# Kernel tuning notes

Hardware: AMD Instinct MI355X
Metric: run time of the kernel (lower is better)

Reference implementation:

```python
import jax, jax.numpy as jnp
import numpy as np

N_CLASSES = 256
PER_CLASS = 128
N_SUPPORT = 5
N_QUERY = PER_CLASS - N_SUPPORT  # 123
N_VIEW = 2
D = 384
N = N_CLASSES * PER_CLASS  # 32768


def setup_inputs() -> dict:
    key = jax.random.key(0)
    k1, k2 = jax.random.split(key, 2)
    reps = jax.random.normal(k1, (N, N_VIEW, D), dtype=jnp.float32)
    # block-sorted labels: class c occupies rows [c*PER_CLASS, (c+1)*PER_CLASS)
    labels = (jnp.arange(N, dtype=jnp.int32) // PER_CLASS).astype(jnp.int32)
    return {"reps": reps, "labels": labels}


def reference(reps, labels):
    # labels are block-sorted per class, so the original's
    # labels.eq(c).nonzero()[:n_support] / [n_support:] gathers are static reshapes.
    reps_r = reps.reshape(N_CLASSES, PER_CLASS, N_VIEW, D)
    # class-mean prototypes over the support set: [C, V, D]
    prototypes = reps_r[:, :N_SUPPORT].mean(axis=1)
    # query samples: [C*N_QUERY, V, D]
    queries = reps_r[:, N_SUPPORT:].reshape(N_CLASSES * N_QUERY, N_VIEW, D)

    x2 = jnp.sum(queries * queries, axis=-1)            # [n, V]
    y2 = jnp.sum(prototypes * prototypes, axis=-1)      # [m, V]
    xy = jnp.einsum('nvd,mvd->nmv', queries, prototypes)  # [n, m, V]
    dists = x2[:, None, :] + y2[None, :, :] - 2.0 * xy

    # log_softmax over the prototype (class) axis
    log_p_y = jax.nn.log_softmax(-dists, axis=1)
    log_p_y = log_p_y.reshape(N_CLASSES, N_QUERY, N_CLASSES, N_VIEW)

    # gather the true-class log-prob for each query / view
    cls = jnp.arange(N_CLASSES)
    correct = log_p_y[cls, :, cls, :]  # [C, N_QUERY, V]
    loss = -correct.mean()
    return loss
```

## Files before the change

### kernel.cpp

```cpp
#include <hip/hip_runtime.h>
#include <hip/hip_bf16.h>
#include <math.h>

#define NCLS 256
#define PER_CLASS 128
#define NSUP 5
#define NQRY 123
#define NVIEW 2
#define DD 384
#define NQ_TOT (NCLS * NQRY)
#define BM 128
#define BK 32
#define NKT (DD / BK)
#define QS 40
#define PS 32

typedef __attribute__((ext_vector_type(8))) short short8;
typedef __attribute__((ext_vector_type(4))) float floatx4;

union FragU { uint4 u; short8 s; };
union PkU { __hip_bfloat162 b2; unsigned int u; };

__device__ __forceinline__ unsigned int cvt2bf(float lo, float hi) {
    PkU p;
    p.b2 = __float22bfloat162_rn(make_float2(lo, hi));
    return p.u;
}

__device__ __forceinline__ void gll16(const ushort* g, ushort* l) {
    __builtin_amdgcn_global_load_lds(
        (const __attribute__((address_space(1))) unsigned int*)g,
        (__attribute__((address_space(3))) unsigned int*)l, 16, 0, 0);
}

#define BARRIER() asm volatile("s_waitcnt lgkmcnt(0)\n\ts_barrier" ::: "memory")
#define WAITVM(n) asm volatile("s_waitcnt vmcnt(" #n ")" ::: "memory")

__global__ __launch_bounds__(384) void proto_kernel(const float* __restrict__ reps,
                                                    ushort* __restrict__ pbf,
                                                    float* __restrict__ y2,
                                                    float* __restrict__ out) {
    __shared__ float wp[6];
    const int b = blockIdx.x;
    const int c = b & 255, v = b >> 8;
    const int d = threadIdx.x;
    if (b == 0 && d == 0) out[0] = 0.f;
    const float* p = reps + ((size_t)(c * PER_CLASS) * NVIEW + v) * DD + d;
    float s = 0.f;
#pragma unroll
    for (int k = 0; k < NSUP; ++k) s += p[(size_t)k * NVIEW * DD];
    s *= 0.2f;
    __hip_bfloat16 h = __float2bfloat16(s);
    pbf[(size_t)b * DD + d] = *reinterpret_cast<ushort*>(&h);
    float q = s * s;
#pragma unroll
    for (int o = 1; o < 64; o <<= 1) q += __shfl_xor(q, o);
    if ((d & 63) == 0) wp[d >> 6] = q;
    __syncthreads();
    if (d == 0) y2[b] = wp[0] + wp[1] + wp[2] + wp[3] + wp[4] + wp[5];
}

__global__ __launch_bounds__(512, 4) void main_kernel(const float* __restrict__ reps,
                                                      const ushort* __restrict__ pbf,
                                                      const float* __restrict__ y2g,
                                                      float* __restrict__ out) {
    __shared__ ushort q_lds[2][BM * QS];
    __shared__ ushort p_lds[2][NCLS * PS];

    const int t = threadIdx.x;
    const int v = blockIdx.y;
    const int q0 = blockIdx.x * BM;
    const int wave = t >> 6;
    const int lane = t & 63;
    const int col = lane & 15;
    const int quad = lane >> 4;
    const int wm = wave >> 2;
    const int wn = wave & 3;

    const int sq = t >> 2;
    const int f8 = (t & 3) * 8;
    const int nq = q0 + sq;
    const float* qsrc = reps +
        (size_t)((nq / NQRY) * PER_CLASS + NSUP + (nq % NQRY)) * (NVIEW * DD) + v * DD + f8;

    const ushort* psrc = pbf + (size_t)(v * NCLS + wave * 32 + (lane >> 2)) * DD
                             + (((lane & 3) ^ ((lane >> 3) & 3)) << 3);

    const int sP = (col >> 1) & 3;
    const int pbase = (wn * 64 + col) * PS + ((quad ^ sP) << 3);

    floatx4 acc[4][4];
#pragma unroll
    for (int mt = 0; mt < 4; ++mt)
#pragma unroll
        for (int nt = 0; nt < 4; ++nt) acc[mt][nt] = (floatx4)0.f;

    float4 qfA[2], qfB[2];

#define LOADQ(kt, R)                                                               \
    do {                                                                           \
        R[0] = *(const float4*)(qsrc + (kt) * BK);                                 \
        R[1] = *(const float4*)(qsrc + (kt) * BK + 4);                             \
    } while (0)

#define GLLP(kt, b)                                                                \
    do {                                                                           \
        gll16(psrc + (kt) * BK, &p_lds[b][wave * 1024]);                           \
        gll16(psrc + 16 * DD + (kt) * BK, &p_lds[b][wave * 1024 + 512]);           \
    } while (0)

#define STAGEQ(b, R)                                                               \
    do {                                                                           \
        uint4 w;                                                                   \
        w.x = cvt2bf(R[0].x, R[0].y); w.y = cvt2bf(R[0].z, R[0].w);                \
        w.z = cvt2bf(R[1].x, R[1].y); w.w = cvt2bf(R[1].z, R[1].w);                \
        *(uint4*)&q_lds[b][sq * QS + f8] = w;                                      \
    } while (0)

#define COMPUTE(b)                                                                 \
    do {                                                                           \
        short8 af[4];                                                              \
        _Pragma("unroll") for (int mt = 0; mt < 4; ++mt) {                         \
            FragU f;                                                               \
            f.u = *(const uint4*)&q_lds[b][(wm * 64 + mt * 16 + col) * QS + quad * 8]; \
            af[mt] = f.s;                                                          \
        }                                                                          \
        _Pragma("unroll") for (int nt = 0; nt < 4; ++nt) {                         \
            FragU bb;                                                              \
            bb.u = *(const uint4*)&p_lds[b][pbase + nt * 16 * PS];                 \
            _Pragma("unroll") for (int mt = 0; mt < 4; ++mt)                       \
                acc[mt][nt] = __builtin_amdgcn_mfma_f32_16x16x32_bf16(af[mt], bb.s, acc[mt][nt], 0, 0, 0); \
        }                                                                          \
    } while (0)

    LOADQ(0, qfA); GLLP(0, 0);
    LOADQ(1, qfB); GLLP(1, 1);
    WAITVM(4);
    STAGEQ(0, qfA);
    BARRIER();

#pragma unroll
    for (int kt = 0; kt < NKT; ++kt) {
        COMPUTE(kt & 1);
        if (kt == NKT - 1) break;
        BARRIER();
        if (kt < NKT - 2) {
            if ((kt & 1) == 0) { LOADQ(kt + 2, qfA); } else { LOADQ(kt + 2, qfB); }
            GLLP(kt + 2, kt & 1);
            WAITVM(4);
        } else {
            WAITVM(0);
        }
        if ((kt & 1) == 0) STAGEQ(1, qfB); else STAGEQ(0, qfA);
        BARRIER();
    }

    __syncthreads();
    float* eplds = (float*)&p_lds[0][0];
    float (*pmx)[4] = (float(*)[4])eplds;
    float (*pse)[4] = (float(*)[4])(eplds + 512);
    float* wred = eplds + 1024;

    float y2c[4];
#pragma unroll
    for (int nt = 0; nt < 4; ++nt) y2c[nt] = y2g[v * NCLS + wn * 64 + nt * 16 + col];

    float corr = 0.f;
#pragma unroll
    for (int mt = 0; mt < 4; ++mt) {
#pragma unroll
        for (int r = 0; r < 4; ++r) {
            const int qloc = wm * 64 + mt * 16 + quad * 4 + r;
            const int n = q0 + qloc;
            const int cn = n / NQRY;
            float s[4];
            float mx = -1e30f;
#pragma unroll
            for (int nt = 0; nt < 4; ++nt) {
                s[nt] = 2.f * acc[mt][nt][r] - y2c[nt];
                mx = fmaxf(mx, s[nt]);
                if (cn == wn * 64 + nt * 16 + col) corr += s[nt];
            }
#pragma unroll
            for (int o = 1; o < 16; o <<= 1) mx = fmaxf(mx, __shfl_xor(mx, o));
            float e = 0.f;
#pragma unroll
            for (int nt = 0; nt < 4; ++nt) e += __expf(s[nt] - mx);
#pragma unroll
            for (int o = 1; o < 16; o <<= 1) e += __shfl_xor(e, o);
            if (col == 0) { pmx[qloc][wn] = mx; pse[qloc][wn] = e; }
        }
    }
#pragma unroll
    for (int o = 1; o < 64; o <<= 1) corr += __shfl_xor(corr, o);
    if (lane == 0) wred[wave] = corr;
    __syncthreads();

    float lval = 0.f;
    if (t < BM) {
        float m0 = pmx[t][0], m1 = pmx[t][1], m2 = pmx[t][2], m3 = pmx[t][3];
        float M = fmaxf(fmaxf(m0, m1), fmaxf(m2, m3));
        float E = pse[t][0] * __expf(m0 - M) + pse[t][1] * __expf(m1 - M) +
                  pse[t][2] * __expf(m2 - M) + pse[t][3] * __expf(m3 - M);
        lval = M + __logf(E);
    }
#pragma unroll
    for (int o = 1; o < 64; o <<= 1) lval += __shfl_xor(lval, o);
    if (lane == 0) wred[8 + wave] = lval;
    __syncthreads();

    if (t == 0) {
        float tot = (wred[8] + wred[9] + wred[10] + wred[11] +
                     wred[12] + wred[13] + wred[14] + wred[15]) -
                    (wred[0] + wred[1] + wred[2] + wred[3] +
                     wred[4] + wred[5] + wred[6] + wred[7]);
        atomicAdd(out, tot * (1.f / (float)(NQ_TOT * NVIEW)));
    }
}

extern "C" void kernel_launch(void* const* d_in, const int* in_sizes, int n_in,
                              void* d_out, int out_size, void* d_ws, size_t ws_size,
                              hipStream_t stream) {
    const float* reps = (const float*)d_in[0];
    float* ws = (float*)d_ws;
    ushort* pbf = (ushort*)ws;
    float* y2 = (float*)(pbf + NVIEW * NCLS * DD);
    float* out = (float*)d_out;

    proto_kernel<<<dim3(NVIEW * NCLS), dim3(DD), 0, stream>>>(reps, pbf, y2, out);
    main_kernel<<<dim3(NQ_TOT / BM, NVIEW), dim3(512), 0, stream>>>(reps, pbf, y2, out);
}
```

Baseline: 165.5 us.

## Pre-convert queries to bf16 and triple-buffer tiles with direct global-to-LDS loads

The prep kernel now also converts every query row from fp32 to a packed bf16 buffer in workspace, alongside computing prototypes. The main kernel loads both query and prototype tiles straight into LDS with global_load_lds and a three-stage buffer, removing the register staging and the conversion from the GEMM loop and one barrier per iteration. In exchange it adds an extra full write and read of the bf16 query copy. It also drops the LDS padding and swizzle, which may cause bank conflicts, and uses more LDS per block, which may lower occupancy.

```diff
diff --git a/kernel.cpp b/kernel.cpp
--- a/kernel.cpp
+++ b/kernel.cpp
@@ -12,8 +12,9 @@
 #define BM 128
 #define BK 32
 #define NKT (DD / BK)
-#define QS 40
-#define PS 32
+#define NPROTO (NVIEW * NCLS)
+#define QCONV_BLOCKS 1536
+#define CHUNKS (NVIEW * NQ_TOT * (DD / 8))
 
 typedef __attribute__((ext_vector_type(8))) short short8;
 typedef __attribute__((ext_vector_type(4))) float floatx4;
@@ -36,36 +37,57 @@
 #define BARRIER() asm volatile("s_waitcnt lgkmcnt(0)\n\ts_barrier" ::: "memory")
 #define WAITVM(n) asm volatile("s_waitcnt vmcnt(" #n ")" ::: "memory")
 
-__global__ __launch_bounds__(384) void proto_kernel(const float* __restrict__ reps,
-                                                    ushort* __restrict__ pbf,
-                                                    float* __restrict__ y2,
-                                                    float* __restrict__ out) {
+__global__ __launch_bounds__(384) void prep_kernel(const float* __restrict__ reps,
+                                                   ushort* __restrict__ pbf,
+                                                   float* __restrict__ y2,
+                                                   ushort* __restrict__ qbf,
+                                                   float* __restrict__ out) {
     __shared__ float wp[6];
-    const int b = blockIdx.x;
-    const int c = b & 255, v = b >> 8;
-    const int d = threadIdx.x;
-    if (b == 0 && d == 0) out[0] = 0.f;
-    const float* p = reps + ((size_t)(c * PER_CLASS) * NVIEW + v) * DD + d;
-    float s = 0.f;
-#pragma unroll
-    for (int k = 0; k < NSUP; ++k) s += p[(size_t)k * NVIEW * DD];
-    s *= 0.2f;
-    __hip_bfloat16 h = __float2bfloat16(s);
-    pbf[(size_t)b * DD + d] = *reinterpret_cast<ushort*>(&h);
-    float q = s * s;
-#pragma unroll
-    for (int o = 1; o < 64; o <<= 1) q += __shfl_xor(q, o);
-    if ((d & 63) == 0) wp[d >> 6] = q;
-    __syncthreads();
-    if (d == 0) y2[b] = wp[0] + wp[1] + wp[2] + wp[3] + wp[4] + wp[5];
-}
-
-__global__ __launch_bounds__(512, 4) void main_kernel(const float* __restrict__ reps,
+    const int t = threadIdx.x;
+    if (blockIdx.x < NPROTO) {
+        const int b = blockIdx.x;
+        const int c = b & 255, v = b >> 8;
+        if (b == 0 && t == 0) out[0] = 0.f;
+        const float* p = reps + ((size_t)(c * PER_CLASS) * NVIEW + v) * DD + t;
+        float s = 0.f;
+#pragma unroll
+        for (int k = 0; k < NSUP; ++k) s += p[(size_t)k * NVIEW * DD];
+        s *= 0.2f;
+        __hip_bfloat16 h = __float2bfloat16(s);
+        pbf[(size_t)b * DD + t] = *reinterpret_cast<ushort*>(&h);
+        float q = s * s;
+#pragma unroll
+        for (int o = 1; o < 64; o <<= 1) q += __shfl_xor(q, o);
+        if ((t & 63) == 0) wp[t >> 6] = q;
+        __syncthreads();
+        if (t == 0) y2[b] = wp[0] + wp[1] + wp[2] + wp[3] + wp[4] + wp[5];
+    } else {
+        const int g0 = (blockIdx.x - NPROTO) * 384 + t;
+        for (int g = g0; g < CHUNKS; g += QCONV_BLOCKS * 384) {
+            const int row = g / 48;
+            const int d8 = g - row * 48;
+            const int v = row / NQ_TOT;
+            const int nq = row - v * NQ_TOT;
+            const int c = nq / NQRY;
+            const int qi = nq - c * NQRY;
+            const float* src = reps +
+                (size_t)((c * PER_CLASS + NSUP + qi) * NVIEW + v) * DD + d8 * 8;
+            const float4 a = *(const float4*)src;
+            const float4 b4 = *(const float4*)(src + 4);
+            uint4 w;
+            w.x = cvt2bf(a.x, a.y);  w.y = cvt2bf(a.z, a.w);
+            w.z = cvt2bf(b4.x, b4.y); w.w = cvt2bf(b4.z, b4.w);
+            *(uint4*)(qbf + (size_t)row * DD + d8 * 8) = w;
+        }
+    }
+}
+
+__global__ __launch_bounds__(512, 4) void main_kernel(const ushort* __restrict__ qbf,
                                                       const ushort* __restrict__ pbf,
                                                       const float* __restrict__ y2g,
                                                       float* __restrict__ out) {
-    __shared__ ushort q_lds[2][BM * QS];
-    __shared__ ushort p_lds[2][NCLS * PS];
+    __shared__ ushort q_lds[3][BM * 32];
+    __shared__ ushort p_lds[3][NCLS * 32];
 
     const int t = threadIdx.x;
     const int v = blockIdx.y;
@@ -77,17 +99,14 @@
     const int wm = wave >> 2;
     const int wn = wave & 3;
 
-    const int sq = t >> 2;
-    const int f8 = (t & 3) * 8;
-    const int nq = q0 + sq;
-    const float* qsrc = reps +
-        (size_t)((nq / NQRY) * PER_CLASS + NSUP + (nq % NQRY)) * (NVIEW * DD) + v * DD + f8;
-
-    const ushort* psrc = pbf + (size_t)(v * NCLS + wave * 32 + (lane >> 2)) * DD
-                             + (((lane & 3) ^ ((lane >> 3) & 3)) << 3);
-
-    const int sP = (col >> 1) & 3;
-    const int pbase = (wn * 64 + col) * PS + ((quad ^ sP) << 3);
+    const ushort* qsrc = qbf + (size_t)(v * NQ_TOT + q0 + wave * 16 + (lane >> 2)) * DD
+                             + (lane & 3) * 8;
+    const ushort* psrc0 = pbf + (size_t)(v * NCLS + wave * 16 + (lane >> 2)) * DD
+                              + (lane & 3) * 8;
+    const ushort* psrc1 = psrc0 + (size_t)128 * DD;
+
+    const int qdst = wave * 512;
+    const int pdst1 = 4096 + wave * 512;
 
     floatx4 acc[4][4];
 #pragma unroll
@@ -95,26 +114,11 @@
 #pragma unroll
         for (int nt = 0; nt < 4; ++nt) acc[mt][nt] = (floatx4)0.f;
 
-    float4 qfA[2], qfB[2];
-
-#define LOADQ(kt, R)                                                               \
+#define GLLT(kt, b)                                                                \
     do {                                                                           \
-        R[0] = *(const float4*)(qsrc + (kt) * BK);                                 \
-        R[1] = *(const float4*)(qsrc + (kt) * BK + 4);                             \
-    } while (0)
-
-#define GLLP(kt, b)                                                                \
-    do {                                                                           \
-        gll16(psrc + (kt) * BK, &p_lds[b][wave * 1024]);                           \
-        gll16(psrc + 16 * DD + (kt) * BK, &p_lds[b][wave * 1024 + 512]);           \
-    } while (0)
-
-#define STAGEQ(b, R)                                                               \
-    do {                                                                           \
-        uint4 w;                                                                   \
-        w.x = cvt2bf(R[0].x, R[0].y); w.y = cvt2bf(R[0].z, R[0].w);                \
-        w.z = cvt2bf(R[1].x, R[1].y); w.w = cvt2bf(R[1].z, R[1].w);                \
-        *(uint4*)&q_lds[b][sq * QS + f8] = w;                                      \
+        gll16(qsrc + (kt) * BK, &q_lds[b][qdst]);                                  \
+        gll16(psrc0 + (kt) * BK, &p_lds[b][qdst]);                                 \
+        gll16(psrc1 + (kt) * BK, &p_lds[b][pdst1]);                                \
     } while (0)
 
 #define COMPUTE(b)                                                                 \
@@ -122,41 +126,34 @@
         short8 af[4];                                                              \
         _Pragma("unroll") for (int mt = 0; mt < 4; ++mt) {                         \
             FragU f;                                                               \
-            f.u = *(const uint4*)&q_lds[b][(wm * 64 + mt * 16 + col) * QS + quad * 8]; \
+            f.u = *(const uint4*)&q_lds[b][(wm * 64 + mt * 16 + col) * 32 + quad * 8]; \
             af[mt] = f.s;                                                          \
         }                                                                          \
         _Pragma("unroll") for (int nt = 0; nt < 4; ++nt) {                         \
             FragU bb;                                                              \
-            bb.u = *(const uint4*)&p_lds[b][pbase + nt * 16 * PS];                 \
+            bb.u = *(const uint4*)&p_lds[b][(wn * 64 + nt * 16 + col) * 32 + quad * 8]; \
             _Pragma("unroll") for (int mt = 0; mt < 4; ++mt)                       \
                 acc[mt][nt] = __builtin_amdgcn_mfma_f32_16x16x32_bf16(af[mt], bb.s, acc[mt][nt], 0, 0, 0); \
         }                                                                          \
     } while (0)
 
-    LOADQ(0, qfA); GLLP(0, 0);
-    LOADQ(1, qfB); GLLP(1, 1);
-    WAITVM(4);
-    STAGEQ(0, qfA);
+    GLLT(0, 0);
+    GLLT(1, 1);
+    GLLT(2, 2);
+    WAITVM(6);
     BARRIER();
 
 #pragma unroll
     for (int kt = 0; kt < NKT; ++kt) {
-        COMPUTE(kt & 1);
+        COMPUTE(kt % 3);
         if (kt == NKT - 1) break;
+        if (kt + 2 < NKT) { WAITVM(3); } else { WAITVM(0); }
         BARRIER();
-        if (kt < NKT - 2) {
-            if ((kt & 1) == 0) { LOADQ(kt + 2, qfA); } else { LOADQ(kt + 2, qfB); }
-            GLLP(kt + 2, kt & 1);
-            WAITVM(4);
-        } else {
-            WAITVM(0);
-        }
-        if ((kt & 1) == 0) STAGEQ(1, qfB); else STAGEQ(0, qfA);
-        BARRIER();
+        if (kt + 3 < NKT) GLLT(kt + 3, kt % 3);
     }
 
     __syncthreads();
-    float* eplds = (float*)&p_lds[0][0];
+    float* eplds = (float*)&q_lds[0][0];
     float (*pmx)[4] = (float(*)[4])eplds;
     float (*pse)[4] = (float(*)[4])(eplds + 512);
     float* wred = eplds + 1024;
@@ -222,11 +219,11 @@
                               void* d_out, int out_size, void* d_ws, size_t ws_size,
                               hipStream_t stream) {
     const float* reps = (const float*)d_in[0];
-    float* ws = (float*)d_ws;
-    ushort* pbf = (ushort*)ws;
+    ushort* pbf = (ushort*)d_ws;
     float* y2 = (float*)(pbf + NVIEW * NCLS * DD);
+    ushort* qbf = (ushort*)(y2 + NVIEW * NCLS);
     float* out = (float*)d_out;
 
-    proto_kernel<<<dim3(NVIEW * NCLS), dim3(DD), 0, stream>>>(reps, pbf, y2, out);
-    main_kernel<<<dim3(NQ_TOT / BM, NVIEW), dim3(512), 0, stream>>>(reps, pbf, y2, out);
-}
+    prep_kernel<<<dim3(NPROTO + QCONV_BLOCKS), dim3(384), 0, stream>>>(reps, pbf, y2, qbf, out);
+    main_kernel<<<dim3(NQ_TOT / BM, NVIEW), dim3(512), 0, stream>>>(qbf, pbf, y2, out);
+}
```

Result: slower. 186.5 us (+12.7%).

## Stage the full query tile into LDS upfront with swizzled layout

Applied to the files above, without the earlier changes.

Each block now loads its whole 128x384 query tile once at the start (24 float4 loads per thread), converts it to bf16 and writes it into a single large LDS buffer with an XOR swizzle. This replaces the per-k-step double-buffered query staging, so the main loop only streams prototype tiles. The aim is to issue all query loads early with high memory-level parallelism and remove per-iteration conversion and LDS-store work. In exchange LDS use grows to about 96KB plus the prototype buffers and register pressure rises, so occupancy drops (launch bounds lowered from 4 to 2) and the query loads are no longer overlapped with the MFMA compute.

```diff
diff --git a/kernel.cpp b/kernel.cpp
--- a/kernel.cpp
+++ b/kernel.cpp
@@ -12,7 +12,6 @@
 #define BM 128
 #define BK 32
 #define NKT (DD / BK)
-#define QS 40
 #define PS 32
 
 typedef __attribute__((ext_vector_type(8))) short short8;
@@ -60,11 +59,11 @@
     if (d == 0) y2[b] = wp[0] + wp[1] + wp[2] + wp[3] + wp[4] + wp[5];
 }
 
-__global__ __launch_bounds__(512, 4) void main_kernel(const float* __restrict__ reps,
+__global__ __launch_bounds__(512, 2) void main_kernel(const float* __restrict__ reps,
                                                       const ushort* __restrict__ pbf,
                                                       const float* __restrict__ y2g,
                                                       float* __restrict__ out) {
-    __shared__ ushort q_lds[2][BM * QS];
+    __shared__ ushort q_lds[NKT * BM * 32];
     __shared__ ushort p_lds[2][NCLS * PS];
 
     const int t = threadIdx.x;
@@ -77,31 +76,11 @@
     const int wm = wave >> 2;
     const int wn = wave & 3;
 
-    const int sq = t >> 2;
-    const int f8 = (t & 3) * 8;
-    const int nq = q0 + sq;
-    const float* qsrc = reps +
-        (size_t)((nq / NQRY) * PER_CLASS + NSUP + (nq % NQRY)) * (NVIEW * DD) + v * DD + f8;
-
     const ushort* psrc = pbf + (size_t)(v * NCLS + wave * 32 + (lane >> 2)) * DD
                              + (((lane & 3) ^ ((lane >> 3) & 3)) << 3);
 
     const int sP = (col >> 1) & 3;
     const int pbase = (wn * 64 + col) * PS + ((quad ^ sP) << 3);
-
-    floatx4 acc[4][4];
-#pragma unroll
-    for (int mt = 0; mt < 4; ++mt)
-#pragma unroll
-        for (int nt = 0; nt < 4; ++nt) acc[mt][nt] = (floatx4)0.f;
-
-    float4 qfA[2], qfB[2];
-
-#define LOADQ(kt, R)                                                               \
-    do {                                                                           \
-        R[0] = *(const float4*)(qsrc + (kt) * BK);                                 \
-        R[1] = *(const float4*)(qsrc + (kt) * BK + 4);                             \
-    } while (0)
 
 #define GLLP(kt, b)                                                                \
     do {                                                                           \
@@ -109,49 +88,73 @@
         gll16(psrc + 16 * DD + (kt) * BK, &p_lds[b][wave * 1024 + 512]);           \
     } while (0)
 
-#define STAGEQ(b, R)                                                               \
-    do {                                                                           \
-        uint4 w;                                                                   \
-        w.x = cvt2bf(R[0].x, R[0].y); w.y = cvt2bf(R[0].z, R[0].w);                \
-        w.z = cvt2bf(R[1].x, R[1].y); w.w = cvt2bf(R[1].z, R[1].w);                \
-        *(uint4*)&q_lds[b][sq * QS + f8] = w;                                      \
-    } while (0)
-
-#define COMPUTE(b)                                                                 \
+    GLLP(0, 0);
+    GLLP(1, 1);
+
+    {
+        const int qrow = t >> 2;
+        const int qp = t & 3;
+        const int nq = q0 + qrow;
+        const float* qsrc = reps +
+            (size_t)((nq / NQRY) * PER_CLASS + NSUP + (nq % NQRY)) * (NVIEW * DD) +
+            v * DD + qp * 96;
+        const int swzq = (qrow >> 1) & 3;
+
+        float4 A[24];
+#pragma unroll
+        for (int i = 0; i < 24; ++i) A[i] = *(const float4*)(qsrc + i * 4);
+#pragma unroll
+        for (int g = 0; g < 3; ++g) {
+            const int kt = qp * 3 + g;
+#pragma unroll
+            for (int q = 0; q < 4; ++q) {
+                uint4 w;
+                w.x = cvt2bf(A[g * 8 + 2 * q].x, A[g * 8 + 2 * q].y);
+                w.y = cvt2bf(A[g * 8 + 2 * q].z, A[g * 8 + 2 * q].w);
+                w.z = cvt2bf(A[g * 8 + 2 * q + 1].x, A[g * 8 + 2 * q + 1].y);
+                w.w = cvt2bf(A[g * 8 + 2 * q + 1].z, A[g * 8 + 2 * q + 1].w);
+                *(uint4*)&q_lds[kt * 4096 + qrow * 32 + ((q ^ swzq) << 3)] = w;
+            }
+        }
+    }
+
+    floatx4 acc[4][4];
+#pragma unroll
+    for (int mt = 0; mt < 4; ++mt)
+#pragma unroll
+        for (int nt = 0; nt < 4; ++nt) acc[mt][nt] = (floatx4)0.f;
+
+#define COMPUTE(kt, pb)                                                            \
     do {                                                                           \
         short8 af[4];                                                              \
         _Pragma("unroll") for (int mt = 0; mt < 4; ++mt) {                         \
             FragU f;                                                               \
-            f.u = *(const uint4*)&q_lds[b][(wm * 64 + mt * 16 + col) * QS + quad * 8]; \
+            f.u = *(const uint4*)&q_lds[(kt) * 4096 +                              \
+                (wm * 64 + mt * 16 + col) * 32 + ((quad ^ sP) << 3)];              \
             af[mt] = f.s;                                                          \
         }                                                                          \
         _Pragma("unroll") for (int nt = 0; nt < 4; ++nt) {                         \
             FragU bb;                                                              \
-            bb.u = *(const uint4*)&p_lds[b][pbase + nt * 16 * PS];                 \
+            bb.u = *(const uint4*)&p_lds[pb][pbase + nt * 16 * PS];                \
             _Pragma("unroll") for (int mt = 0; mt < 4; ++mt)                       \
                 acc[mt][nt] = __builtin_amdgcn_mfma_f32_16x16x32_bf16(af[mt], bb.s, acc[mt][nt], 0, 0, 0); \
         }                                                                          \
     } while (0)
 
-    LOADQ(0, qfA); GLLP(0, 0);
-    LOADQ(1, qfB); GLLP(1, 1);
-    WAITVM(4);
-    STAGEQ(0, qfA);
+    WAITVM(0);
     BARRIER();
 
 #pragma unroll
     for (int kt = 0; kt < NKT; ++kt) {
-        COMPUTE(kt & 1);
+        COMPUTE(kt, kt & 1);
         if (kt == NKT - 1) break;
         BARRIER();
-        if (kt < NKT - 2) {
-            if ((kt & 1) == 0) { LOADQ(kt + 2, qfA); } else { LOADQ(kt + 2, qfB); }
+        if (kt + 2 < NKT) {
             GLLP(kt + 2, kt & 1);
-            WAITVM(4);
+            WAITVM(2);
         } else {
             WAITVM(0);
         }
-        if ((kt & 1) == 0) STAGEQ(1, qfB); else STAGEQ(0, qfA);
         BARRIER();
     }
 
```

Measured after the change: 177.8 us. +7.4%, slower.
